# Optimization experiments

Hardware: AMD Instinct MI355X
Metric: run time of the kernel (lower is better)

The kernel has to match this reference:

```python
import jax, jax.numpy as jnp
import numpy as np

BATCH, DIM = 8192, 1024  # batch of ODE states, state dimension (orig dim=100 scaled up)
ETA = 1.0                # self.eta
B_DECAY = 1.0            # self.B (linear decay coefficient)


def setup_inputs() -> dict:
    key = jax.random.key(0)
    k1, k2, k3, k4, k5 = jax.random.split(key, 5)
    return {
        "x":      jax.random.normal(k1, (BATCH, DIM), jnp.float32),
        "e_x":    jax.random.normal(k2, (BATCH, DIM), jnp.float32),
        "W":      jax.random.normal(k3, (BATCH, DIM), jnp.float32),
        "A":      jax.random.normal(k4, (DIM, DIM), jnpp := jnp.float32) / np.float32(np.sqrt(DIM)),
        "target": jax.random.normal(k5, (1, DIM), jnp.float32),
    }


def reference(x, e_x, W, A, target):
    # b_ast = diagonal of B_ast = diag(target^2 / (1 + target^2)); mm with a diag
    # matrix == elementwise multiply by its diagonal.  [1, D]
    b_ast = target ** 2 / (1.0 + target ** 2)
    # control: u = -eta * (W * (x + e_x - target)) @ B_ast              [B, D]
    u = -ETA * (W * ((x + e_x) - target)) * b_ast
    # saturating nonlinearity sigma(x) = x^2 / (1 + x^2)                [B, D]
    sig = x ** 2 / (1.0 + x ** 2)
    # dx = -B*x + A @ sigma(x) (per state: sigma(x) @ A^T) + u*sigma(x) [B, D]
    dx = -B_DECAY * x + sig @ A.T + u * sig
    # original returns tuple(dx_i) + tuple(-dx_i) + tuple(zeros): stack as [3, B, D]
    return jnp.stack([dx, -dx, jnp.zeros_like(dx)])
```

## Files before the change

kernel.cpp:

```cpp
#include <hip/hip_runtime.h>
#include <stdint.h>

#define BATCH 8192
#define DIM   1024
#define BM 128
#define BN 128
#define BK 64
#define NT (DIM / BK)

typedef __attribute__((ext_vector_type(4))) float f32x4;
typedef __attribute__((ext_vector_type(8))) short bf16x8;
typedef __attribute__((ext_vector_type(4))) unsigned short u16x4;
typedef __attribute__((ext_vector_type(8))) unsigned short u16x8;

#define AS1(p) ((const __attribute__((address_space(1))) void*)(p))
#define AS3(p) ((__attribute__((address_space(3))) void*)(p))

__device__ __forceinline__ unsigned short f2bf(float f) {
    union { float f; unsigned int u; } v; v.f = f;
    unsigned int u = v.u;
    u += 0x7fffu + ((u >> 16) & 1u);
    return (unsigned short)(u >> 16);
}

__device__ __forceinline__ float sigma_f(float x) {
    float x2 = x * x;
    return x2 * __builtin_amdgcn_rcpf(1.0f + x2);
}

__global__ __launch_bounds__(256) void convA_kernel(
    const float* __restrict__ A, unsigned short* __restrict__ Ab)
{
    int idx = blockIdx.x * 256 + threadIdx.x;
    f32x4 av = ((const f32x4*)A)[idx];
    u16x4 ab;
#pragma unroll
    for (int i = 0; i < 4; ++i) ab[i] = f2bf(av[i]);
    ((u16x4*)Ab)[idx] = ab;
}

__global__ __launch_bounds__(512, 4) void fused_kernel(
    const float* __restrict__ x, const float* __restrict__ ex,
    const float* __restrict__ W, const float* __restrict__ tgt,
    const unsigned short* __restrict__ Ab,
    float* __restrict__ out0, float* __restrict__ out1,
    float* __restrict__ out2)
{
    __shared__ __align__(16) char lds[65536];

    const int p    = blockIdx.x;
    const int xcd  = p & 7;
    const int slot = p >> 3;
    const int bm   = xcd * 8 + (slot >> 3);
    const int bn   = slot & 7;

    const int tid  = threadIdx.x;
    const int lane = tid & 63;
    const int wid  = tid >> 6;
    const int wr   = wid >> 2;
    const int wc   = wid & 3;

    const int swz = (((lane & 7) ^ (lane >> 3)) << 4);
    const char* gB = (const char*)Ab +
        ((size_t)(bn * BN + (lane >> 3)) * DIM) * 2 + swz;

    const int r0 = tid >> 3;
    const int g  = tid & 7;
    const float* gx = x + (size_t)(bm * BM + r0) * DIM + g * 8;
    const int wAoff = (g * 16) ^ ((r0 & 7) << 4);

    const int rd_sw = (lane & 7) << 4;
    const int cb0   = (lane >> 4) << 4;

    f32x4 acc[4][2];
#pragma unroll
    for (int mi = 0; mi < 4; ++mi)
#pragma unroll
        for (int ni = 0; ni < 2; ++ni)
            acc[mi][ni] = f32x4{0.f, 0.f, 0.f, 0.f};

    {
        f32x4 xa[2][2];
#pragma unroll
        for (int s = 0; s < 2; ++s) {
            xa[s][0] = *(const f32x4*)(gx + (size_t)s * 64 * DIM);
            xa[s][1] = *(const f32x4*)(gx + (size_t)s * 64 * DIM + 4);
        }
        char* dstB = lds + 16384;
#pragma unroll
        for (int j = 0; j < 2; ++j)
            __builtin_amdgcn_global_load_lds(
                AS1(gB + (size_t)(j * 64 + wid * 8) * (DIM * 2)),
                AS3(dstB + (j * 64 + wid * 8) * 128), 16, 0, 0);
#pragma unroll
        for (int s = 0; s < 2; ++s) {
            u16x8 sb;
#pragma unroll
            for (int i = 0; i < 4; ++i) {
                sb[i]     = f2bf(sigma_f(xa[s][0][i]));
                sb[i + 4] = f2bf(sigma_f(xa[s][1][i]));
            }
            *(u16x8*)(lds + (s * 64 + r0) * 128 + wAoff) = sb;
        }
    }
    __syncthreads();

    for (int t = 0; t < NT; ++t) {
        const int cur = t & 1;
        f32x4 xa[2][2];
        if (t + 1 < NT) {
            const int k0n = (t + 1) * BK;
#pragma unroll
            for (int s = 0; s < 2; ++s) {
                xa[s][0] = *(const f32x4*)(gx + (size_t)s * 64 * DIM + k0n);
                xa[s][1] = *(const f32x4*)(gx + (size_t)s * 64 * DIM + k0n + 4);
            }
            char* dstB = lds + (cur ^ 1) * 32768 + 16384;
#pragma unroll
            for (int j = 0; j < 2; ++j)
                __builtin_amdgcn_global_load_lds(
                    AS1(gB + (size_t)(j * 64 + wid * 8) * (DIM * 2) + (size_t)k0n * 2),
                    AS3(dstB + (j * 64 + wid * 8) * 128), 16, 0, 0);
        }
        __builtin_amdgcn_sched_barrier(0);

        const char* As_ = lds + cur * 32768;
        const char* Bs_ = As_ + 16384;
#pragma unroll
        for (int kk = 0; kk < 2; ++kk) {
            bf16x8 af[4], bfr[2];
#pragma unroll
            for (int mi = 0; mi < 4; ++mi)
                af[mi] = *(const bf16x8*)(As_ + (wr * 64 + mi * 16 + (lane & 15)) * 128 +
                                          ((cb0 + kk * 64) ^ rd_sw));
#pragma unroll
            for (int ni = 0; ni < 2; ++ni)
                bfr[ni] = *(const bf16x8*)(Bs_ + (wc * 32 + ni * 16 + (lane & 15)) * 128 +
                                           ((cb0 + kk * 64) ^ rd_sw));
#pragma unroll
            for (int mi = 0; mi < 4; ++mi)
#pragma unroll
                for (int ni = 0; ni < 2; ++ni)
                    acc[mi][ni] = __builtin_amdgcn_mfma_f32_16x16x32_bf16(
                        af[mi], bfr[ni], acc[mi][ni], 0, 0, 0);
        }
        __builtin_amdgcn_sched_barrier(0);

        if (t + 1 < NT) {
            char* dstA = lds + (cur ^ 1) * 32768;
#pragma unroll
            for (int s = 0; s < 2; ++s) {
                u16x8 sb;
#pragma unroll
                for (int i = 0; i < 4; ++i) {
                    sb[i]     = f2bf(sigma_f(xa[s][0][i]));
                    sb[i + 4] = f2bf(sigma_f(xa[s][1][i]));
                }
                *(u16x8*)(dstA + (s * 64 + r0) * 128 + wAoff) = sb;
            }
        }
        __syncthreads();
    }

#pragma unroll
    for (int mi = 0; mi < 4; ++mi)
#pragma unroll
        for (int ni = 0; ni < 2; ++ni) {
            const int row_ = wr * 64 + mi * 16 + ((lane >> 4) << 2);
            const int colb = (wc * 32 + ni * 16 + (lane & 15)) * 4;
#pragma unroll
            for (int r = 0; r < 4; ++r) {
                const int rr = row_ + r;
                *(float*)(lds + rr * 512 + (colb ^ (((rr >> 2) & 7) << 4))) = acc[mi][ni][r];
            }
        }
    __syncthreads();

#pragma unroll
    for (int i = 0; i < 8; ++i) {
        const int ci  = tid + i * 512;
        const int row = ci >> 5;
        const int cv  = ci & 31;
        f32x4 c = *(const f32x4*)(lds + row * 512 + ((cv * 16) ^ (((row >> 2) & 7) << 4)));
        const size_t v4 = (size_t)(bm * BM + row) * (DIM / 4) + bn * (BN / 4) + cv;
        f32x4 xv = ((const f32x4*)x)[v4];
        f32x4 ev = ((const f32x4*)ex)[v4];
        f32x4 wv = ((const f32x4*)W)[v4];
        f32x4 tv = ((const f32x4*)tgt)[bn * (BN / 4) + cv];
        f32x4 o0;
#pragma unroll
        for (int e = 0; e < 4; ++e) {
            float xi = xv[e], ti = tv[e];
            float ba = ti * ti * __builtin_amdgcn_rcpf(1.0f + ti * ti);
            float u  = -(wv[e] * (xi + ev[e] - ti)) * ba;
            float s  = sigma_f(xi);
            o0[e] = -xi + u * s + c[e];
        }
        ((f32x4*)out0)[v4] = o0;
        ((f32x4*)out1)[v4] = -o0;
        ((f32x4*)out2)[v4] = f32x4{0.f, 0.f, 0.f, 0.f};
    }
}

extern "C" void kernel_launch(void* const* d_in, const int* in_sizes, int n_in,
                              void* d_out, int out_size, void* d_ws, size_t ws_size,
                              hipStream_t stream)
{
    const float* x   = (const float*)d_in[0];
    const float* ex  = (const float*)d_in[1];
    const float* W   = (const float*)d_in[2];
    const float* A   = (const float*)d_in[3];
    const float* tgt = (const float*)d_in[4];

    float* out0 = (float*)d_out;
    float* out1 = out0 + (size_t)BATCH * DIM;
    float* out2 = out1 + (size_t)BATCH * DIM;

    unsigned short* Abf = (unsigned short*)d_ws;

    convA_kernel<<<DIM * DIM / 4 / 256, 256, 0, stream>>>(A, Abf);
    fused_kernel<<<(BATCH / BM) * (DIM / BN), 512, 0, stream>>>(
        x, ex, W, tgt, Abf, out0, out1, out2);
}
```

Baseline: 61.17 us.

## Process two N-tiles per block and overlap epilogue with next tile's GEMM

Each block now computes two adjacent 128-column output tiles in sequence. The first tile's epilogue (elementwise math and out0/out1 stores) is spread across the second tile's K-loop, and the zero-fill of out2 is spread across the first loop, so stores overlap with MFMA work. The grid is halved and LDS doubles to 128KB for a separate C staging buffer, which lowers occupancy to 2 blocks per CU. The bf16 conversion now uses the HIP intrinsic type.

```diff
diff --git a/kernel.cpp b/kernel.cpp
--- a/kernel.cpp
+++ b/kernel.cpp
@@ -1,4 +1,5 @@
 #include <hip/hip_runtime.h>
+#include <hip/hip_bf16.h>
 #include <stdint.h>
 
 #define BATCH 8192
@@ -17,10 +18,9 @@
 #define AS3(p) ((__attribute__((address_space(3))) void*)(p))
 
 __device__ __forceinline__ unsigned short f2bf(float f) {
-    union { float f; unsigned int u; } v; v.f = f;
-    unsigned int u = v.u;
-    u += 0x7fffu + ((u >> 16) & 1u);
-    return (unsigned short)(u >> 16);
+    union { __hip_bfloat16 h; unsigned short u; } v;
+    v.h = __hip_bfloat16(f);
+    return v.u;
 }
 
 __device__ __forceinline__ float sigma_f(float x) {
@@ -39,30 +39,33 @@
     ((u16x4*)Ab)[idx] = ab;
 }
 
-__global__ __launch_bounds__(512, 4) void fused_kernel(
+__global__ __launch_bounds__(512, 2) void fused_kernel(
     const float* __restrict__ x, const float* __restrict__ ex,
     const float* __restrict__ W, const float* __restrict__ tgt,
     const unsigned short* __restrict__ Ab,
     float* __restrict__ out0, float* __restrict__ out1,
     float* __restrict__ out2)
 {
-    __shared__ __align__(16) char lds[65536];
-
-    const int p    = blockIdx.x;
-    const int xcd  = p & 7;
-    const int slot = p >> 3;
-    const int bm   = xcd * 8 + (slot >> 3);
-    const int bn   = slot & 7;
+    __shared__ __align__(16) char lds[131072];
+    char* Cl = lds + 65536;
+
+    const int b     = blockIdx.x;
+    const int xcd   = b & 7;
+    const int local = b >> 3;
+    const int bm    = xcd * 8 + (local >> 2);
+    const int bn0   = (local & 3) * 2;
+    const int bn1   = bn0 + 1;
 
     const int tid  = threadIdx.x;
     const int lane = tid & 63;
     const int wid  = tid >> 6;
     const int wr   = wid >> 2;
     const int wc   = wid & 3;
+    const int l15  = lane & 15;
 
     const int swz = (((lane & 7) ^ (lane >> 3)) << 4);
-    const char* gB = (const char*)Ab +
-        ((size_t)(bn * BN + (lane >> 3)) * DIM) * 2 + swz;
+    const char* gBb = (const char*)Ab +
+        ((size_t)(wid * 8 + (lane >> 3)) * DIM) * 2 + swz;
 
     const int r0 = tid >> 3;
     const int g  = tid & 7;
@@ -73,25 +76,23 @@
     const int cb0   = (lane >> 4) << 4;
 
     f32x4 acc[4][2];
-#pragma unroll
-    for (int mi = 0; mi < 4; ++mi)
-#pragma unroll
-        for (int ni = 0; ni < 2; ++ni)
-            acc[mi][ni] = f32x4{0.f, 0.f, 0.f, 0.f};
-
-    {
-        f32x4 xa[2][2];
-#pragma unroll
-        for (int s = 0; s < 2; ++s) {
-            xa[s][0] = *(const f32x4*)(gx + (size_t)s * 64 * DIM);
-            xa[s][1] = *(const f32x4*)(gx + (size_t)s * 64 * DIM + 4);
-        }
-        char* dstB = lds + 16384;
+
+    auto stageB = [&](int bn, int k, char* Bs) {
+        const char* gB = gBb + (size_t)bn * (BN * DIM * 2) + (size_t)k * 2;
 #pragma unroll
         for (int j = 0; j < 2; ++j)
             __builtin_amdgcn_global_load_lds(
-                AS1(gB + (size_t)(j * 64 + wid * 8) * (DIM * 2)),
-                AS3(dstB + (j * 64 + wid * 8) * 128), 16, 0, 0);
+                AS1(gB + (size_t)j * (64 * DIM * 2)),
+                AS3(Bs + (wid * 8 + j * 64) * 128), 16, 0, 0);
+    };
+    auto loadX = [&](int k, f32x4 xa[2][2]) {
+#pragma unroll
+        for (int s = 0; s < 2; ++s) {
+            xa[s][0] = *(const f32x4*)(gx + (size_t)s * 64 * DIM + k);
+            xa[s][1] = *(const f32x4*)(gx + (size_t)s * 64 * DIM + k + 4);
+        }
+    };
+    auto writeSig = [&](char* As, f32x4 xa[2][2]) {
 #pragma unroll
         for (int s = 0; s < 2; ++s) {
             u16x8 sb;
@@ -100,42 +101,22 @@
                 sb[i]     = f2bf(sigma_f(xa[s][0][i]));
                 sb[i + 4] = f2bf(sigma_f(xa[s][1][i]));
             }
-            *(u16x8*)(lds + (s * 64 + r0) * 128 + wAoff) = sb;
-        }
-    }
-    __syncthreads();
-
-    for (int t = 0; t < NT; ++t) {
-        const int cur = t & 1;
-        f32x4 xa[2][2];
-        if (t + 1 < NT) {
-            const int k0n = (t + 1) * BK;
-#pragma unroll
-            for (int s = 0; s < 2; ++s) {
-                xa[s][0] = *(const f32x4*)(gx + (size_t)s * 64 * DIM + k0n);
-                xa[s][1] = *(const f32x4*)(gx + (size_t)s * 64 * DIM + k0n + 4);
-            }
-            char* dstB = lds + (cur ^ 1) * 32768 + 16384;
-#pragma unroll
-            for (int j = 0; j < 2; ++j)
-                __builtin_amdgcn_global_load_lds(
-                    AS1(gB + (size_t)(j * 64 + wid * 8) * (DIM * 2) + (size_t)k0n * 2),
-                    AS3(dstB + (j * 64 + wid * 8) * 128), 16, 0, 0);
-        }
-        __builtin_amdgcn_sched_barrier(0);
-
-        const char* As_ = lds + cur * 32768;
-        const char* Bs_ = As_ + 16384;
+            *(u16x8*)(As + (r0 + s * 64) * 128 + wAoff) = sb;
+        }
+    };
+    auto mfmaPhase = [&](const char* buf) {
+        const char* As_ = buf;
+        const char* Bs_ = buf + 16384;
 #pragma unroll
         for (int kk = 0; kk < 2; ++kk) {
             bf16x8 af[4], bfr[2];
 #pragma unroll
             for (int mi = 0; mi < 4; ++mi)
-                af[mi] = *(const bf16x8*)(As_ + (wr * 64 + mi * 16 + (lane & 15)) * 128 +
+                af[mi] = *(const bf16x8*)(As_ + (wr * 64 + mi * 16 + l15) * 128 +
                                           ((cb0 + kk * 64) ^ rd_sw));
 #pragma unroll
             for (int ni = 0; ni < 2; ++ni)
-                bfr[ni] = *(const bf16x8*)(Bs_ + (wc * 32 + ni * 16 + (lane & 15)) * 128 +
+                bfr[ni] = *(const bf16x8*)(Bs_ + (wc * 32 + ni * 16 + l15) * 128 +
                                            ((cb0 + kk * 64) ^ rd_sw));
 #pragma unroll
             for (int mi = 0; mi < 4; ++mi)
@@ -144,61 +125,139 @@
                     acc[mi][ni] = __builtin_amdgcn_mfma_f32_16x16x32_bf16(
                         af[mi], bfr[ni], acc[mi][ni], 0, 0, 0);
         }
-        __builtin_amdgcn_sched_barrier(0);
-
+    };
+    auto dumpC = [&]() {
+#pragma unroll
+        for (int mi = 0; mi < 4; ++mi)
+#pragma unroll
+            for (int ni = 0; ni < 2; ++ni) {
+                const int row_ = wr * 64 + mi * 16 + ((lane >> 4) << 2);
+                const int colb = (wc * 32 + ni * 16 + l15) * 4;
+#pragma unroll
+                for (int r = 0; r < 4; ++r) {
+                    const int rr = row_ + r;
+                    *(float*)(Cl + rr * 512 + (colb ^ (((rr >> 2) & 7) << 4))) = acc[mi][ni][r];
+                }
+            }
+    };
+
+#pragma unroll
+    for (int mi = 0; mi < 4; ++mi)
+#pragma unroll
+        for (int ni = 0; ni < 2; ++ni)
+            acc[mi][ni] = f32x4{0.f, 0.f, 0.f, 0.f};
+
+    {
+        f32x4 xa[2][2];
+        loadX(0, xa);
+        stageB(bn0, 0, lds + 16384);
+        writeSig(lds, xa);
+    }
+    __syncthreads();
+
+    for (int t = 0; t < NT; ++t) {
+        const int cur = t & 1;
+        f32x4 xa[2][2];
         if (t + 1 < NT) {
-            char* dstA = lds + (cur ^ 1) * 32768;
-#pragma unroll
-            for (int s = 0; s < 2; ++s) {
-                u16x8 sb;
-#pragma unroll
-                for (int i = 0; i < 4; ++i) {
-                    sb[i]     = f2bf(sigma_f(xa[s][0][i]));
-                    sb[i + 4] = f2bf(sigma_f(xa[s][1][i]));
-                }
-                *(u16x8*)(dstA + (s * 64 + r0) * 128 + wAoff) = sb;
+            loadX((t + 1) * BK, xa);
+            stageB(bn0, (t + 1) * BK, lds + (cur ^ 1) * 32768 + 16384);
+        }
+        {
+            const int j = t * 512 + tid;
+            const int tile = j >> 12;
+            const int v = j & 4095;
+            const size_t v4 = (size_t)(bm * BM + (v >> 5)) * (DIM / 4) +
+                              (bn0 + tile) * 32 + (v & 31);
+            ((f32x4*)out2)[v4] = f32x4{0.f, 0.f, 0.f, 0.f};
+        }
+        __builtin_amdgcn_sched_barrier(0);
+        mfmaPhase(lds + cur * 32768);
+        __builtin_amdgcn_sched_barrier(0);
+        if (t + 1 < NT) writeSig(lds + (cur ^ 1) * 32768, xa);
+        __syncthreads();
+    }
+
+    dumpC();
+#pragma unroll
+    for (int mi = 0; mi < 4; ++mi)
+#pragma unroll
+        for (int ni = 0; ni < 2; ++ni)
+            acc[mi][ni] = f32x4{0.f, 0.f, 0.f, 0.f};
+    {
+        f32x4 xa[2][2];
+        loadX(0, xa);
+        stageB(bn1, 0, lds + 16384);
+        writeSig(lds, xa);
+    }
+    __syncthreads();
+
+    for (int t = 0; t < NT; ++t) {
+        const int cur = t & 1;
+        f32x4 xa[2][2];
+        if (t + 1 < NT) {
+            loadX((t + 1) * BK, xa);
+            stageB(bn1, (t + 1) * BK, lds + (cur ^ 1) * 32768 + 16384);
+        }
+        f32x4 eC, eX, eE, eW, eT;
+        size_t ev4 = 0;
+        const bool doEpi = (t & 1);
+        if (doEpi) {
+            const int p  = t >> 1;
+            const int ci = tid + p * 512;
+            const int row = ci >> 5;
+            const int cv  = ci & 31;
+            eC = *(const f32x4*)(Cl + row * 512 + ((cv * 16) ^ (((row >> 2) & 7) << 4)));
+            ev4 = (size_t)(bm * BM + row) * (DIM / 4) + bn0 * 32 + cv;
+            eX = ((const f32x4*)x)[ev4];
+            eE = ((const f32x4*)ex)[ev4];
+            eW = ((const f32x4*)W)[ev4];
+            eT = ((const f32x4*)tgt)[bn0 * 32 + cv];
+        }
+        __builtin_amdgcn_sched_barrier(0);
+        mfmaPhase(lds + cur * 32768);
+        __builtin_amdgcn_sched_barrier(0);
+        if (t + 1 < NT) writeSig(lds + (cur ^ 1) * 32768, xa);
+        if (doEpi) {
+            f32x4 o0;
+#pragma unroll
+            for (int e = 0; e < 4; ++e) {
+                float xi = eX[e], ti = eT[e];
+                float ba = ti * ti * __builtin_amdgcn_rcpf(1.0f + ti * ti);
+                float u  = -(eW[e] * (xi + eE[e] - ti)) * ba;
+                float s  = sigma_f(xi);
+                o0[e] = -xi + u * s + eC[e];
             }
+            ((f32x4*)out0)[ev4] = o0;
+            ((f32x4*)out1)[ev4] = -o0;
         }
         __syncthreads();
     }
 
-#pragma unroll
-    for (int mi = 0; mi < 4; ++mi)
-#pragma unroll
-        for (int ni = 0; ni < 2; ++ni) {
-            const int row_ = wr * 64 + mi * 16 + ((lane >> 4) << 2);
-            const int colb = (wc * 32 + ni * 16 + (lane & 15)) * 4;
-#pragma unroll
-            for (int r = 0; r < 4; ++r) {
-                const int rr = row_ + r;
-                *(float*)(lds + rr * 512 + (colb ^ (((rr >> 2) & 7) << 4))) = acc[mi][ni][r];
-            }
-        }
+    dumpC();
     __syncthreads();
 
 #pragma unroll
-    for (int i = 0; i < 8; ++i) {
-        const int ci  = tid + i * 512;
+    for (int p = 0; p < 8; ++p) {
+        const int ci = tid + p * 512;
         const int row = ci >> 5;
         const int cv  = ci & 31;
-        f32x4 c = *(const f32x4*)(lds + row * 512 + ((cv * 16) ^ (((row >> 2) & 7) << 4)));
-        const size_t v4 = (size_t)(bm * BM + row) * (DIM / 4) + bn * (BN / 4) + cv;
+        f32x4 c = *(const f32x4*)(Cl + row * 512 + ((cv * 16) ^ (((row >> 2) & 7) << 4)));
+        const size_t v4 = (size_t)(bm * BM + row) * (DIM / 4) + bn1 * 32 + cv;
         f32x4 xv = ((const f32x4*)x)[v4];
-        f32x4 ev = ((const f32x4*)ex)[v4];
+        f32x4 evv = ((const f32x4*)ex)[v4];
         f32x4 wv = ((const f32x4*)W)[v4];
-        f32x4 tv = ((const f32x4*)tgt)[bn * (BN / 4) + cv];
+        f32x4 tv = ((const f32x4*)tgt)[bn1 * 32 + cv];
         f32x4 o0;
 #pragma unroll
         for (int e = 0; e < 4; ++e) {
             float xi = xv[e], ti = tv[e];
             float ba = ti * ti * __builtin_amdgcn_rcpf(1.0f + ti * ti);
-            float u  = -(wv[e] * (xi + ev[e] - ti)) * ba;
+            float u  = -(wv[e] * (xi + evv[e] - ti)) * ba;
             float s  = sigma_f(xi);
             o0[e] = -xi + u * s + c[e];
         }
         ((f32x4*)out0)[v4] = o0;
         ((f32x4*)out1)[v4] = -o0;
-        ((f32x4*)out2)[v4] = f32x4{0.f, 0.f, 0.f, 0.f};
     }
 }
 
@@ -219,6 +278,6 @@
     unsigned short* Abf = (unsigned short*)d_ws;
 
     convA_kernel<<<DIM * DIM / 4 / 256, 256, 0, stream>>>(A, Abf);
-    fused_kernel<<<(BATCH / BM) * (DIM / BN), 512, 0, stream>>>(
+    fused_kernel<<<(BATCH / BM) * (DIM / BN) / 2, 512, 0, stream>>>(
         x, ex, W, tgt, Abf, out0, out1, out2);
 }
```

New measurement: 62.93 us. 1.03x slower.

## Shrink GEMM tiles to 64x64 with 256-thread blocks and remap XCD scheduling

Applied to the files above, without the earlier changes.

Halves the block tile to 64x64 with four waves of 2x2 MFMA fragments per wave, halves LDS to 32KB and raises the occupancy hint. Blocks are remapped so each XCD covers 16 row-tiles across 16 column-tiles, and bf16 conversion now uses the HIP intrinsic type. The aim is more blocks and higher occupancy to hide latency, at the cost of less reuse per tile: the sigmoid of x is recomputed for 16 column tiles instead of 8, and A is reloaded more often. The epilogue LDS layout also drops its XOR swizzle, which may bring bank conflicts.

```diff
diff --git a/kernel.cpp b/kernel.cpp
--- a/kernel.cpp
+++ b/kernel.cpp
@@ -1,10 +1,11 @@
 #include <hip/hip_runtime.h>
+#include <hip/hip_bf16.h>
 #include <stdint.h>
 
 #define BATCH 8192
 #define DIM   1024
-#define BM 128
-#define BN 128
+#define BM 64
+#define BN 64
 #define BK 64
 #define NT (DIM / BK)
 
@@ -17,10 +18,9 @@
 #define AS3(p) ((__attribute__((address_space(3))) void*)(p))
 
 __device__ __forceinline__ unsigned short f2bf(float f) {
-    union { float f; unsigned int u; } v; v.f = f;
-    unsigned int u = v.u;
-    u += 0x7fffu + ((u >> 16) & 1u);
-    return (unsigned short)(u >> 16);
+    union { __hip_bfloat16 h; unsigned short u; } v;
+    v.h = __hip_bfloat16(f);
+    return v.u;
 }
 
 __device__ __forceinline__ float sigma_f(float x) {
@@ -39,30 +39,31 @@
     ((u16x4*)Ab)[idx] = ab;
 }
 
-__global__ __launch_bounds__(512, 4) void fused_kernel(
+__global__ __launch_bounds__(256, 5) void fused_kernel(
     const float* __restrict__ x, const float* __restrict__ ex,
     const float* __restrict__ W, const float* __restrict__ tgt,
     const unsigned short* __restrict__ Ab,
     float* __restrict__ out0, float* __restrict__ out1,
     float* __restrict__ out2)
 {
-    __shared__ __align__(16) char lds[65536];
-
-    const int p    = blockIdx.x;
-    const int xcd  = p & 7;
-    const int slot = p >> 3;
-    const int bm   = xcd * 8 + (slot >> 3);
-    const int bn   = slot & 7;
+    __shared__ __align__(16) char lds[32768];
+
+    const int b     = blockIdx.x;
+    const int xcd   = b & 7;
+    const int local = b >> 3;
+    const int bm    = xcd * 16 + (local >> 4);
+    const int bn    = local & 15;
 
     const int tid  = threadIdx.x;
     const int lane = tid & 63;
     const int wid  = tid >> 6;
-    const int wr   = wid >> 2;
-    const int wc   = wid & 3;
+    const int wr   = wid >> 1;
+    const int wc   = wid & 1;
+    const int l15  = lane & 15;
 
     const int swz = (((lane & 7) ^ (lane >> 3)) << 4);
-    const char* gB = (const char*)Ab +
-        ((size_t)(bn * BN + (lane >> 3)) * DIM) * 2 + swz;
+    const char* gBb = (const char*)Ab +
+        ((size_t)(bn * BN + wid * 16 + (lane >> 3)) * DIM) * 2 + swz;
 
     const int r0 = tid >> 3;
     const int g  = tid & 7;
@@ -72,26 +73,28 @@
     const int rd_sw = (lane & 7) << 4;
     const int cb0   = (lane >> 4) << 4;
 
-    f32x4 acc[4][2];
-#pragma unroll
-    for (int mi = 0; mi < 4; ++mi)
+    f32x4 acc[2][2];
+#pragma unroll
+    for (int mi = 0; mi < 2; ++mi)
 #pragma unroll
         for (int ni = 0; ni < 2; ++ni)
             acc[mi][ni] = f32x4{0.f, 0.f, 0.f, 0.f};
 
-    {
-        f32x4 xa[2][2];
-#pragma unroll
-        for (int s = 0; s < 2; ++s) {
-            xa[s][0] = *(const f32x4*)(gx + (size_t)s * 64 * DIM);
-            xa[s][1] = *(const f32x4*)(gx + (size_t)s * 64 * DIM + 4);
-        }
-        char* dstB = lds + 16384;
+    auto stageB = [&](int k, char* Bs) {
 #pragma unroll
         for (int j = 0; j < 2; ++j)
             __builtin_amdgcn_global_load_lds(
-                AS1(gB + (size_t)(j * 64 + wid * 8) * (DIM * 2)),
-                AS3(dstB + (j * 64 + wid * 8) * 128), 16, 0, 0);
+                AS1(gBb + (size_t)j * (8 * DIM * 2) + (size_t)k * 2),
+                AS3(Bs + (wid * 16 + j * 8) * 128), 16, 0, 0);
+    };
+    auto loadX = [&](int k, f32x4 xa[2][2]) {
+#pragma unroll
+        for (int s = 0; s < 2; ++s) {
+            xa[s][0] = *(const f32x4*)(gx + (size_t)s * 32 * DIM + k);
+            xa[s][1] = *(const f32x4*)(gx + (size_t)s * 32 * DIM + k + 4);
+        }
+    };
+    auto writeSig = [&](char* As, f32x4 xa[2][2]) {
 #pragma unroll
         for (int s = 0; s < 2; ++s) {
             u16x8 sb;
@@ -100,8 +103,15 @@
                 sb[i]     = f2bf(sigma_f(xa[s][0][i]));
                 sb[i + 4] = f2bf(sigma_f(xa[s][1][i]));
             }
-            *(u16x8*)(lds + (s * 64 + r0) * 128 + wAoff) = sb;
-        }
+            *(u16x8*)(As + (r0 + s * 32) * 128 + wAoff) = sb;
+        }
+    };
+
+    {
+        f32x4 xa[2][2];
+        loadX(0, xa);
+        stageB(0, lds + 8192);
+        writeSig(lds, xa);
     }
     __syncthreads();
 
@@ -109,36 +119,26 @@
         const int cur = t & 1;
         f32x4 xa[2][2];
         if (t + 1 < NT) {
-            const int k0n = (t + 1) * BK;
-#pragma unroll
-            for (int s = 0; s < 2; ++s) {
-                xa[s][0] = *(const f32x4*)(gx + (size_t)s * 64 * DIM + k0n);
-                xa[s][1] = *(const f32x4*)(gx + (size_t)s * 64 * DIM + k0n + 4);
-            }
-            char* dstB = lds + (cur ^ 1) * 32768 + 16384;
-#pragma unroll
-            for (int j = 0; j < 2; ++j)
-                __builtin_amdgcn_global_load_lds(
-                    AS1(gB + (size_t)(j * 64 + wid * 8) * (DIM * 2) + (size_t)k0n * 2),
-                    AS3(dstB + (j * 64 + wid * 8) * 128), 16, 0, 0);
+            loadX((t + 1) * BK, xa);
+            stageB((t + 1) * BK, lds + (cur ^ 1) * 16384 + 8192);
         }
         __builtin_amdgcn_sched_barrier(0);
 
-        const char* As_ = lds + cur * 32768;
-        const char* Bs_ = As_ + 16384;
+        const char* As_ = lds + cur * 16384;
+        const char* Bs_ = As_ + 8192;
 #pragma unroll
         for (int kk = 0; kk < 2; ++kk) {
-            bf16x8 af[4], bfr[2];
-#pragma unroll
-            for (int mi = 0; mi < 4; ++mi)
-                af[mi] = *(const bf16x8*)(As_ + (wr * 64 + mi * 16 + (lane & 15)) * 128 +
+            bf16x8 af[2], bfr[2];
+#pragma unroll
+            for (int mi = 0; mi < 2; ++mi)
+                af[mi] = *(const bf16x8*)(As_ + (wr * 32 + mi * 16 + l15) * 128 +
                                           ((cb0 + kk * 64) ^ rd_sw));
 #pragma unroll
             for (int ni = 0; ni < 2; ++ni)
-                bfr[ni] = *(const bf16x8*)(Bs_ + (wc * 32 + ni * 16 + (lane & 15)) * 128 +
+                bfr[ni] = *(const bf16x8*)(Bs_ + (wc * 32 + ni * 16 + l15) * 128 +
                                            ((cb0 + kk * 64) ^ rd_sw));
 #pragma unroll
-            for (int mi = 0; mi < 4; ++mi)
+            for (int mi = 0; mi < 2; ++mi)
 #pragma unroll
                 for (int ni = 0; ni < 2; ++ni)
                     acc[mi][ni] = __builtin_amdgcn_mfma_f32_16x16x32_bf16(
@@ -146,42 +146,28 @@
         }
         __builtin_amdgcn_sched_barrier(0);
 
-        if (t + 1 < NT) {
-            char* dstA = lds + (cur ^ 1) * 32768;
-#pragma unroll
-            for (int s = 0; s < 2; ++s) {
-                u16x8 sb;
-#pragma unroll
-                for (int i = 0; i < 4; ++i) {
-                    sb[i]     = f2bf(sigma_f(xa[s][0][i]));
-                    sb[i + 4] = f2bf(sigma_f(xa[s][1][i]));
-                }
-                *(u16x8*)(dstA + (s * 64 + r0) * 128 + wAoff) = sb;
-            }
-        }
+        if (t + 1 < NT) writeSig(lds + (cur ^ 1) * 16384, xa);
         __syncthreads();
     }
 
 #pragma unroll
-    for (int mi = 0; mi < 4; ++mi)
+    for (int mi = 0; mi < 2; ++mi)
 #pragma unroll
         for (int ni = 0; ni < 2; ++ni) {
-            const int row_ = wr * 64 + mi * 16 + ((lane >> 4) << 2);
-            const int colb = (wc * 32 + ni * 16 + (lane & 15)) * 4;
-#pragma unroll
-            for (int r = 0; r < 4; ++r) {
-                const int rr = row_ + r;
-                *(float*)(lds + rr * 512 + (colb ^ (((rr >> 2) & 7) << 4))) = acc[mi][ni][r];
-            }
+            const int row_ = wr * 32 + mi * 16 + ((lane >> 4) << 2);
+            const int colb = (wc * 32 + ni * 16 + l15) * 4;
+#pragma unroll
+            for (int r = 0; r < 4; ++r)
+                *(float*)(lds + (row_ + r) * 256 + colb) = acc[mi][ni][r];
         }
     __syncthreads();
 
 #pragma unroll
-    for (int i = 0; i < 8; ++i) {
-        const int ci  = tid + i * 512;
-        const int row = ci >> 5;
-        const int cv  = ci & 31;
-        f32x4 c = *(const f32x4*)(lds + row * 512 + ((cv * 16) ^ (((row >> 2) & 7) << 4)));
+    for (int p = 0; p < 4; ++p) {
+        const int ci  = tid + p * 256;
+        const int row = ci >> 4;
+        const int cv  = ci & 15;
+        f32x4 c = *(const f32x4*)(lds + row * 256 + cv * 16);
         const size_t v4 = (size_t)(bm * BM + row) * (DIM / 4) + bn * (BN / 4) + cv;
         f32x4 xv = ((const f32x4*)x)[v4];
         f32x4 ev = ((const f32x4*)ex)[v4];
@@ -219,6 +205,6 @@
     unsigned short* Abf = (unsigned short*)d_ws;
 
     convA_kernel<<<DIM * DIM / 4 / 256, 256, 0, stream>>>(A, Abf);
-    fused_kernel<<<(BATCH / BM) * (DIM / BN), 512, 0, stream>>>(
+    fused_kernel<<<(BATCH / BM) * (DIM / BN), 256, 0, stream>>>(
         x, ex, W, tgt, Abf, out0, out1, out2);
 }
```

Result: slower. 65.63 us (+7.3%).

## Warp-specialize GEMM into MFMA waves and producer waves that prefetch epilogue inputs

Applied to the files above, without the earlier changes.

Splits the 8 waves into 4 compute waves that only issue MFMAs and 4 producer waves. The producer waves load the next A/x tiles, compute sigma into LDS, and gradually load and precompute the elementwise epilogue term (-x + u*sigma) into a separate LDS region during the K loop. The N tile is halved to 64, doubling the grid, and the bf16 conversion now uses the HIP intrinsic. This aims to hide global loads and epilogue work behind the matrix math. In exchange, x is read once per N tile, so twice as often, and only half the waves do MFMA.

```diff
diff --git a/kernel.cpp b/kernel.cpp
--- a/kernel.cpp
+++ b/kernel.cpp
@@ -1,12 +1,13 @@
 #include <hip/hip_runtime.h>
+#include <hip/hip_bf16.h>
 #include <stdint.h>
 
 #define BATCH 8192
 #define DIM   1024
 #define BM 128
-#define BN 128
+#define BN 64
 #define BK 64
-#define NT (DIM / BK)
+#define NT 16
 
 typedef __attribute__((ext_vector_type(4))) float f32x4;
 typedef __attribute__((ext_vector_type(8))) short bf16x8;
@@ -17,10 +18,9 @@
 #define AS3(p) ((__attribute__((address_space(3))) void*)(p))
 
 __device__ __forceinline__ unsigned short f2bf(float f) {
-    union { float f; unsigned int u; } v; v.f = f;
-    unsigned int u = v.u;
-    u += 0x7fffu + ((u >> 16) & 1u);
-    return (unsigned short)(u >> 16);
+    union { __hip_bfloat16 h; unsigned short u; } v;
+    v.h = __hip_bfloat16(f);
+    return v.u;
 }
 
 __device__ __forceinline__ float sigma_f(float x) {
@@ -46,31 +46,19 @@
     float* __restrict__ out0, float* __restrict__ out1,
     float* __restrict__ out2)
 {
-    __shared__ __align__(16) char lds[65536];
-
-    const int p    = blockIdx.x;
-    const int xcd  = p & 7;
-    const int slot = p >> 3;
-    const int bm   = xcd * 8 + (slot >> 3);
-    const int bn   = slot & 7;
+    __shared__ __align__(16) char lds[81920];
+    char* baseL = lds + 49152;
+
+    const int b     = blockIdx.x;
+    const int xcd   = b & 7;
+    const int local = b >> 3;
+    const int bm    = xcd * 8 + (local >> 4);
+    const int bn    = local & 15;
 
     const int tid  = threadIdx.x;
     const int lane = tid & 63;
     const int wid  = tid >> 6;
-    const int wr   = wid >> 2;
-    const int wc   = wid & 3;
-
-    const int swz = (((lane & 7) ^ (lane >> 3)) << 4);
-    const char* gB = (const char*)Ab +
-        ((size_t)(bn * BN + (lane >> 3)) * DIM) * 2 + swz;
-
-    const int r0 = tid >> 3;
-    const int g  = tid & 7;
-    const float* gx = x + (size_t)(bm * BM + r0) * DIM + g * 8;
-    const int wAoff = (g * 16) ^ ((r0 & 7) << 4);
-
-    const int rd_sw = (lane & 7) << 4;
-    const int cb0   = (lane >> 4) << 4;
+    const int l15  = lane & 15;
 
     f32x4 acc[4][2];
 #pragma unroll
@@ -79,123 +67,160 @@
         for (int ni = 0; ni < 2; ++ni)
             acc[mi][ni] = f32x4{0.f, 0.f, 0.f, 0.f};
 
-    {
-        f32x4 xa[2][2];
-#pragma unroll
-        for (int s = 0; s < 2; ++s) {
-            xa[s][0] = *(const f32x4*)(gx + (size_t)s * 64 * DIM);
-            xa[s][1] = *(const f32x4*)(gx + (size_t)s * 64 * DIM + 4);
-        }
-        char* dstB = lds + 16384;
+    f32x4 bx = {}, bev = {}, bwv = {};
+
+    if (wid >= 4) {
+        const int sw  = wid - 4;
+        const int st  = tid - 256;
+        const int swz = (((lane & 7) ^ (lane >> 3)) << 4);
+        const char* gB0 = (const char*)Ab +
+            ((size_t)(bn * BN + sw * 16 + (lane >> 3)) * DIM) * 2 + swz;
 #pragma unroll
         for (int j = 0; j < 2; ++j)
             __builtin_amdgcn_global_load_lds(
-                AS1(gB + (size_t)(j * 64 + wid * 8) * (DIM * 2)),
-                AS3(dstB + (j * 64 + wid * 8) * 128), 16, 0, 0);
-#pragma unroll
-        for (int s = 0; s < 2; ++s) {
+                AS1(gB0 + (size_t)j * (8 * DIM * 2)),
+                AS3(lds + 16384 + (sw * 16 + j * 8) * 128), 16, 0, 0);
+#pragma unroll
+        for (int a = 0; a < 4; ++a) {
+            const int idx = a * 256 + st;
+            const int row = idx >> 3, g = idx & 7;
+            const float* gxs = x + (size_t)(bm * BM + row) * DIM + g * 8;
+            f32x4 v0 = *(const f32x4*)gxs;
+            f32x4 v1 = *(const f32x4*)(gxs + 4);
             u16x8 sb;
 #pragma unroll
             for (int i = 0; i < 4; ++i) {
-                sb[i]     = f2bf(sigma_f(xa[s][0][i]));
-                sb[i + 4] = f2bf(sigma_f(xa[s][1][i]));
-            }
-            *(u16x8*)(lds + (s * 64 + r0) * 128 + wAoff) = sb;
+                sb[i]     = f2bf(sigma_f(v0[i]));
+                sb[i + 4] = f2bf(sigma_f(v1[i]));
+            }
+            *(u16x8*)(lds + row * 128 + ((g * 16) ^ ((row & 7) << 4))) = sb;
         }
     }
     __syncthreads();
 
     for (int t = 0; t < NT; ++t) {
-        const int cur = t & 1;
-        f32x4 xa[2][2];
-        if (t + 1 < NT) {
-            const int k0n = (t + 1) * BK;
-#pragma unroll
-            for (int s = 0; s < 2; ++s) {
-                xa[s][0] = *(const f32x4*)(gx + (size_t)s * 64 * DIM + k0n);
-                xa[s][1] = *(const f32x4*)(gx + (size_t)s * 64 * DIM + k0n + 4);
-            }
-            char* dstB = lds + (cur ^ 1) * 32768 + 16384;
-#pragma unroll
-            for (int j = 0; j < 2; ++j)
-                __builtin_amdgcn_global_load_lds(
-                    AS1(gB + (size_t)(j * 64 + wid * 8) * (DIM * 2) + (size_t)k0n * 2),
-                    AS3(dstB + (j * 64 + wid * 8) * 128), 16, 0, 0);
+        if (wid < 4) {
+            const int wr = wid >> 1, wc = wid & 1;
+            const int rd_sw = (lane & 7) << 4;
+            const int cb0   = (lane >> 4) << 4;
+            const char* As_ = lds + (t & 1) * 24576;
+            const char* Bs_ = As_ + 16384;
+#pragma unroll
+            for (int kk = 0; kk < 2; ++kk) {
+                bf16x8 af[4], bfr[2];
+#pragma unroll
+                for (int mi = 0; mi < 4; ++mi)
+                    af[mi] = *(const bf16x8*)(As_ + (wr * 64 + mi * 16 + l15) * 128 +
+                                              ((cb0 + kk * 64) ^ rd_sw));
+#pragma unroll
+                for (int ni = 0; ni < 2; ++ni)
+                    bfr[ni] = *(const bf16x8*)(Bs_ + (wc * 32 + ni * 16 + l15) * 128 +
+                                               ((cb0 + kk * 64) ^ rd_sw));
+#pragma unroll
+                for (int mi = 0; mi < 4; ++mi)
+#pragma unroll
+                    for (int ni = 0; ni < 2; ++ni)
+                        acc[mi][ni] = __builtin_amdgcn_mfma_f32_16x16x32_bf16(
+                            af[mi], bfr[ni], acc[mi][ni], 0, 0, 0);
+            }
+        } else {
+            const int sw  = wid - 4;
+            const int st  = tid - 256;
+            char* nbuf = lds + ((t + 1) & 1) * 24576;
+            const int kn = (t + 1) * BK;
+
+            if (t + 1 < NT) {
+                const int swz = (((lane & 7) ^ (lane >> 3)) << 4);
+                const char* gB = (const char*)Ab +
+                    ((size_t)(bn * BN + sw * 16 + (lane >> 3)) * DIM) * 2 + swz +
+                    (size_t)kn * 2;
+#pragma unroll
+                for (int j = 0; j < 2; ++j)
+                    __builtin_amdgcn_global_load_lds(
+                        AS1(gB + (size_t)j * (8 * DIM * 2)),
+                        AS3(nbuf + 16384 + (sw * 16 + j * 8) * 128), 16, 0, 0);
+            }
+            __builtin_amdgcn_sched_barrier(0);
+
+            f32x4 xs[4][2];
+            if (t + 1 < NT) {
+#pragma unroll
+                for (int a = 0; a < 4; ++a) {
+                    const int idx = a * 256 + st;
+                    const int row = idx >> 3, g = idx & 7;
+                    const float* gxs = x + (size_t)(bm * BM + row) * DIM + g * 8 + kn;
+                    xs[a][0] = *(const f32x4*)gxs;
+                    xs[a][1] = *(const f32x4*)(gxs + 4);
+                }
+            }
+
+            const int p   = t >> 1;
+            const int row = p * 16 + (st >> 4);
+            const int cv  = st & 15;
+            const size_t v4 = (size_t)(bm * BM + row) * (DIM / 4) + bn * 16 + cv;
+            if (!(t & 1)) {
+                bx  = ((const f32x4*)x)[v4];
+                bev = ((const f32x4*)ex)[v4];
+                bwv = ((const f32x4*)W)[v4];
+            } else {
+                f32x4 tv = ((const f32x4*)tgt)[bn * 16 + cv];
+                f32x4 bq;
+#pragma unroll
+                for (int e = 0; e < 4; ++e) {
+                    float xi = bx[e], ti = tv[e];
+                    float ba = ti * ti * __builtin_amdgcn_rcpf(1.0f + ti * ti);
+                    float u  = -(bwv[e] * (xi + bev[e] - ti)) * ba;
+                    float s  = sigma_f(xi);
+                    bq[e] = -xi + u * s;
+                }
+                *(f32x4*)(baseL + row * 256 + cv * 16) = bq;
+            }
+
+            if (t + 1 < NT) {
+#pragma unroll
+                for (int a = 0; a < 4; ++a) {
+                    const int idx = a * 256 + st;
+                    const int arow = idx >> 3, g = idx & 7;
+                    u16x8 sb;
+#pragma unroll
+                    for (int i = 0; i < 4; ++i) {
+                        sb[i]     = f2bf(sigma_f(xs[a][0][i]));
+                        sb[i + 4] = f2bf(sigma_f(xs[a][1][i]));
+                    }
+                    *(u16x8*)(nbuf + arow * 128 + ((g * 16) ^ ((arow & 7) << 4))) = sb;
+                }
+            }
         }
+        asm volatile("s_waitcnt lgkmcnt(0)" ::: "memory");
         __builtin_amdgcn_sched_barrier(0);
-
-        const char* As_ = lds + cur * 32768;
-        const char* Bs_ = As_ + 16384;
-#pragma unroll
-        for (int kk = 0; kk < 2; ++kk) {
-            bf16x8 af[4], bfr[2];
-#pragma unroll
-            for (int mi = 0; mi < 4; ++mi)
-                af[mi] = *(const bf16x8*)(As_ + (wr * 64 + mi * 16 + (lane & 15)) * 128 +
-                                          ((cb0 + kk * 64) ^ rd_sw));
-#pragma unroll
-            for (int ni = 0; ni < 2; ++ni)
-                bfr[ni] = *(const bf16x8*)(Bs_ + (wc * 32 + ni * 16 + (lane & 15)) * 128 +
-                                           ((cb0 + kk * 64) ^ rd_sw));
-#pragma unroll
-            for (int mi = 0; mi < 4; ++mi)
-#pragma unroll
-                for (int ni = 0; ni < 2; ++ni)
-                    acc[mi][ni] = __builtin_amdgcn_mfma_f32_16x16x32_bf16(
-                        af[mi], bfr[ni], acc[mi][ni], 0, 0, 0);
-        }
+        __builtin_amdgcn_s_barrier();
         __builtin_amdgcn_sched_barrier(0);
-
-        if (t + 1 < NT) {
-            char* dstA = lds + (cur ^ 1) * 32768;
-#pragma unroll
-            for (int s = 0; s < 2; ++s) {
-                u16x8 sb;
-#pragma unroll
-                for (int i = 0; i < 4; ++i) {
-                    sb[i]     = f2bf(sigma_f(xa[s][0][i]));
-                    sb[i + 4] = f2bf(sigma_f(xa[s][1][i]));
-                }
-                *(u16x8*)(dstA + (s * 64 + r0) * 128 + wAoff) = sb;
-            }
-        }
-        __syncthreads();
-    }
-
-#pragma unroll
-    for (int mi = 0; mi < 4; ++mi)
-#pragma unroll
-        for (int ni = 0; ni < 2; ++ni) {
-            const int row_ = wr * 64 + mi * 16 + ((lane >> 4) << 2);
-            const int colb = (wc * 32 + ni * 16 + (lane & 15)) * 4;
-#pragma unroll
-            for (int r = 0; r < 4; ++r) {
-                const int rr = row_ + r;
-                *(float*)(lds + rr * 512 + (colb ^ (((rr >> 2) & 7) << 4))) = acc[mi][ni][r];
-            }
-        }
+    }
+
+    if (wid < 4) {
+        const int wr = wid >> 1, wc = wid & 1;
+#pragma unroll
+        for (int mi = 0; mi < 4; ++mi)
+#pragma unroll
+            for (int ni = 0; ni < 2; ++ni) {
+                const int row_ = wr * 64 + mi * 16 + ((lane >> 4) << 2);
+                const int col  = wc * 32 + ni * 16 + l15;
+#pragma unroll
+                for (int r = 0; r < 4; ++r)
+                    *(float*)(lds + (row_ + r) * 256 + col * 4) = acc[mi][ni][r];
+            }
+    }
     __syncthreads();
 
 #pragma unroll
-    for (int i = 0; i < 8; ++i) {
-        const int ci  = tid + i * 512;
-        const int row = ci >> 5;
-        const int cv  = ci & 31;
-        f32x4 c = *(const f32x4*)(lds + row * 512 + ((cv * 16) ^ (((row >> 2) & 7) << 4)));
-        const size_t v4 = (size_t)(bm * BM + row) * (DIM / 4) + bn * (BN / 4) + cv;
-        f32x4 xv = ((const f32x4*)x)[v4];
-        f32x4 ev = ((const f32x4*)ex)[v4];
-        f32x4 wv = ((const f32x4*)W)[v4];
-        f32x4 tv = ((const f32x4*)tgt)[bn * (BN / 4) + cv];
-        f32x4 o0;
-#pragma unroll
-        for (int e = 0; e < 4; ++e) {
-            float xi = xv[e], ti = tv[e];
-            float ba = ti * ti * __builtin_amdgcn_rcpf(1.0f + ti * ti);
-            float u  = -(wv[e] * (xi + ev[e] - ti)) * ba;
-            float s  = sigma_f(xi);
-            o0[e] = -xi + u * s + c[e];
-        }
+    for (int i = 0; i < 4; ++i) {
+        const int q   = i * 512 + tid;
+        const int row = q >> 4;
+        const int cv  = q & 15;
+        f32x4 c  = *(const f32x4*)(lds  + row * 256 + cv * 16);
+        f32x4 bq = *(const f32x4*)(baseL + row * 256 + cv * 16);
+        const size_t v4 = (size_t)(bm * BM + row) * (DIM / 4) + bn * 16 + cv;
+        f32x4 o0 = bq + c;
         ((f32x4*)out0)[v4] = o0;
         ((f32x4*)out1)[v4] = -o0;
         ((f32x4*)out2)[v4] = f32x4{0.f, 0.f, 0.f, 0.f};
```

After: 76.26 us. 24.7% more time.
